# Optimization experiments

Hardware: AMD Instinct MI355X
Metric: run time of the kernel (lower is better)

Reference implementation:

```python
import jax, jax.numpy as jnp
import numpy as np

GRID_BOUND = 0.5
GRID_SIZE = 64


def _reflect(points, p):
    # points: [B, N, 3], p: [B, 4] plane (a, b, c, d) -> reflect about ax+by+cz+d=0
    n = p[:, :3]                                   # [B, 3]
    d = p[:, 3]                                    # [B]
    denom = jnp.sum(n * n, axis=-1) + 1e-12        # [B]
    t = (jnp.einsum('bnc,bc->bn', points, n) + d[:, None]) / denom[:, None]  # [B, N]
    return points - 2.0 * t[..., None] * n[:, None, :]


def _rotate(points, q):
    # points: [B, N, 3], q: [B, 4] quaternion (w, x, y, z), normalized here
    q = q / (jnp.linalg.norm(q, axis=-1, keepdims=True) + 1e-12)
    w = q[:, 0][:, None, None]                     # [B, 1, 1]
    v = q[:, 1:][:, None, :]                       # [B, 1, 3]
    uv = jnp.cross(v, points)                      # [B, N, 3]
    return points + 2.0 * jnp.cross(v, uv + w * points)


def _cal_distance(pts, cp):
    # pts: [B, N, 3]; cp: [B, G^3, 3] nearest-surface-point per voxel cell
    gs = GRID_SIZE
    # map [-gridBound, gridBound] -> voxel index in [0, gs-1]
    idx = jnp.clip(jnp.floor((pts / (2.0 * GRID_BOUND) + 0.5) * gs), 0, gs - 1).astype(jnp.int32)
    flat = (idx[..., 0] * gs + idx[..., 1]) * gs + idx[..., 2]   # [B, N]
    nearest = jnp.take_along_axis(cp, flat[..., None], axis=1)   # [B, N, 3] irregular gather
    return jnp.mean(jnp.sum((pts - nearest) ** 2, axis=-1))


def setup_inputs() -> dict:
    key = jax.random.key(0)
    k1, k2, k3, k4, k5 = jax.random.split(key, 5)
    B, N, K, gs = 128, 8192, 3, GRID_SIZE
    points = jax.random.uniform(k1, (B, N, 3), jnp.float32) - 0.5   # in [-0.5, 0.5]
    cp = jax.random.uniform(k2, (B, gs ** 3, 3), jnp.float32) - 0.5
    voxel = jax.random.uniform(k3, (B, gs, gs, gs), jnp.float32)
    plane = jax.random.normal(k4, (K, B, 4), jnp.float32)
    quat = jax.random.normal(k5, (K, B, 4), jnp.float32)
    return {"points": points, "cp": cp, "voxel": voxel, "plane": plane, "quat": quat}


def reference(points, cp, voxel, plane, quat):
    # voxel is carried for API fidelity (used only by the custom backward in the
    # original CUDA op); forward math depends on points/cp/plane/quat.
    del voxel
    # vectorize across all K symmetries instead of the original Python loop
    ref_pts = jax.vmap(_reflect, in_axes=(None, 0))(points, plane)  # [K, B, N, 3]
    rot_pts = jax.vmap(_rotate, in_axes=(None, 0))(points, quat)    # [K, B, N, 3]
    ref_loss = jnp.sum(jax.vmap(_cal_distance, in_axes=(0, None))(ref_pts, cp))
    rot_loss = jnp.sum(jax.vmap(_cal_distance, in_axes=(0, None))(rot_pts, cp))
    return ref_loss, rot_loss
```

## Files before the change

kernel.cpp:

```cpp
#include <hip/hip_runtime.h>

#define GS 64
#define BB 128
#define NN 8192
#define KK 3
#define SLICE_FLOATS (GS * GS * GS * 3)
#define B_PER_XCD 16
#define BLOCKS_PER_B 32
#define GRID (BB * BLOCKS_PER_B)

__global__ __launch_bounds__(256) void symloss_main(
    const float* __restrict__ points, const float* __restrict__ cp,
    const float* __restrict__ plane, const float* __restrict__ quat,
    float2* __restrict__ partials) {
    int raw = blockIdx.x;
    int xcd = raw & 7;
    int s   = raw >> 3;
    int b   = xcd * B_PER_XCD + s / BLOCKS_PER_B;
    int chunk = s % BLOCKS_PER_B;
    int n = chunk * 256 + threadIdx.x;

    const float* p = points + ((size_t)b * NN + n) * 3;
    float px = p[0], py = p[1], pz = p[2];
    const float* cpb = cp + (size_t)b * SLICE_FLOATS;

    float tx[2 * KK], ty[2 * KK], tz[2 * KK];

#pragma unroll
    for (int k = 0; k < KK; ++k) {
        const float* plk = plane + ((size_t)k * BB + b) * 4;
        float nx = plk[0], ny = plk[1], nz = plk[2], d = plk[3];
        float denom = nx * nx + ny * ny + nz * nz + 1e-12f;
        float tt = (px * nx + py * ny + pz * nz + d) / denom;
        tx[k] = px - 2.0f * tt * nx;
        ty[k] = py - 2.0f * tt * ny;
        tz[k] = pz - 2.0f * tt * nz;

        const float* q = quat + ((size_t)k * BB + b) * 4;
        float qw = q[0], qx = q[1], qy = q[2], qz = q[3];
        float qn = sqrtf(qw * qw + qx * qx + qy * qy + qz * qz) + 1e-12f;
        qw /= qn; qx /= qn; qy /= qn; qz /= qn;
        float ux = qy * pz - qz * py;
        float uy = qz * px - qx * pz;
        float uz = qx * py - qy * px;
        float sx = ux + qw * px;
        float sy = uy + qw * py;
        float sz = uz + qw * pz;
        tx[KK + k] = px + 2.0f * (qy * sz - qz * sy);
        ty[KK + k] = py + 2.0f * (qz * sx - qx * sz);
        tz[KK + k] = pz + 2.0f * (qx * sy - qy * sx);
    }

    const float* cptr[2 * KK];
#pragma unroll
    for (int i = 0; i < 2 * KK; ++i) {
        float fx = fminf(fmaxf(floorf((tx[i] + 0.5f) * 64.0f), 0.0f), 63.0f);
        float fy = fminf(fmaxf(floorf((ty[i] + 0.5f) * 64.0f), 0.0f), 63.0f);
        float fz = fminf(fmaxf(floorf((tz[i] + 0.5f) * 64.0f), 0.0f), 63.0f);
        int flat = (((int)fx * GS) + (int)fy) * GS + (int)fz;
        cptr[i] = cpb + (size_t)flat * 3;
    }
    float cx[2 * KK], cy[2 * KK], cz[2 * KK];
#pragma unroll
    for (int i = 0; i < 2 * KK; ++i) {
        cx[i] = cptr[i][0];
        cy[i] = cptr[i][1];
        cz[i] = cptr[i][2];
    }

    float ref_acc = 0.0f, rot_acc = 0.0f;
#pragma unroll
    for (int i = 0; i < KK; ++i) {
        float dx = tx[i] - cx[i], dy = ty[i] - cy[i], dz = tz[i] - cz[i];
        ref_acc += dx * dx + dy * dy + dz * dz;
    }
#pragma unroll
    for (int i = KK; i < 2 * KK; ++i) {
        float dx = tx[i] - cx[i], dy = ty[i] - cy[i], dz = tz[i] - cz[i];
        rot_acc += dx * dx + dy * dy + dz * dz;
    }

    for (int off = 32; off > 0; off >>= 1) {
        ref_acc += __shfl_down(ref_acc, off, 64);
        rot_acc += __shfl_down(rot_acc, off, 64);
    }
    __shared__ float s_ref[4], s_rot[4];
    int wave = threadIdx.x >> 6;
    int lane = threadIdx.x & 63;
    if (lane == 0) {
        s_ref[wave] = ref_acc;
        s_rot[wave] = rot_acc;
    }
    __syncthreads();
    if (threadIdx.x == 0) {
        float2 v;
        v.x = s_ref[0] + s_ref[1] + s_ref[2] + s_ref[3];
        v.y = s_rot[0] + s_rot[1] + s_rot[2] + s_rot[3];
        partials[blockIdx.x] = v;
    }
}

__global__ __launch_bounds__(1024) void finalize_kernel(
    const float2* __restrict__ partials, float* __restrict__ out) {
    double r = 0.0, o = 0.0;
    for (int i = threadIdx.x; i < GRID; i += 1024) {
        float2 v = partials[i];
        r += (double)v.x;
        o += (double)v.y;
    }
    __shared__ double s_r[1024], s_o[1024];
    s_r[threadIdx.x] = r;
    s_o[threadIdx.x] = o;
    __syncthreads();
    for (int off = 512; off > 0; off >>= 1) {
        if (threadIdx.x < off) {
            s_r[threadIdx.x] += s_r[threadIdx.x + off];
            s_o[threadIdx.x] += s_o[threadIdx.x + off];
        }
        __syncthreads();
    }
    if (threadIdx.x == 0) {
        const double inv = 1.0 / ((double)BB * (double)NN);
        out[0] = (float)(s_r[0] * inv);
        out[1] = (float)(s_o[0] * inv);
    }
}

extern "C" void kernel_launch(void* const* d_in, const int* in_sizes, int n_in,
                              void* d_out, int out_size, void* d_ws, size_t ws_size,
                              hipStream_t stream) {
    const float* points = (const float*)d_in[0];
    const float* cp     = (const float*)d_in[1];
    const float* plane  = (const float*)d_in[3];
    const float* quat   = (const float*)d_in[4];
    float* out = (float*)d_out;
    float2* partials = (float2*)d_ws;

    symloss_main<<<GRID, 256, 0, stream>>>(points, cp, plane, quat, partials);
    finalize_kernel<<<1, 1024, 0, stream>>>(partials, out);
}
```

Baseline: 62.30 us.

## Process two points per thread and fuse final reduction via last-block atomic

Each thread now handles two points, giving twelve independent gathers in flight per thread while halving the grid. The separate finalize kernel is removed; the last block to finish, detected with an atomic counter, reduces the partials. This removes a kernel launch and raises per-thread memory-level parallelism, at the cost of a memset launch, more registers and fewer blocks.

```diff
diff --git a/kernel.cpp b/kernel.cpp
--- a/kernel.cpp
+++ b/kernel.cpp
@@ -6,63 +6,76 @@
 #define KK 3
 #define SLICE_FLOATS (GS * GS * GS * 3)
 #define B_PER_XCD 16
-#define BLOCKS_PER_B 32
+#define BLOCKS_PER_B 16
 #define GRID (BB * BLOCKS_PER_B)
+#define NSTREAM 12
 
 __global__ __launch_bounds__(256) void symloss_main(
     const float* __restrict__ points, const float* __restrict__ cp,
     const float* __restrict__ plane, const float* __restrict__ quat,
-    float2* __restrict__ partials) {
+    float2* __restrict__ partials, unsigned* __restrict__ ctr,
+    float* __restrict__ out) {
     int raw = blockIdx.x;
     int xcd = raw & 7;
     int s   = raw >> 3;
     int b   = xcd * B_PER_XCD + s / BLOCKS_PER_B;
     int chunk = s % BLOCKS_PER_B;
-    int n = chunk * 256 + threadIdx.x;
+    int n0 = chunk * 512 + threadIdx.x;
 
-    const float* p = points + ((size_t)b * NN + n) * 3;
-    float px = p[0], py = p[1], pz = p[2];
     const float* cpb = cp + (size_t)b * SLICE_FLOATS;
 
-    float tx[2 * KK], ty[2 * KK], tz[2 * KK];
+    float px[2], py[2], pz[2];
+#pragma unroll
+    for (int t = 0; t < 2; ++t) {
+        const float* p = points + ((size_t)b * NN + n0 + t * 256) * 3;
+        px[t] = p[0]; py[t] = p[1]; pz[t] = p[2];
+    }
+
+    float tx[NSTREAM], ty[NSTREAM], tz[NSTREAM];
 
 #pragma unroll
     for (int k = 0; k < KK; ++k) {
         const float* plk = plane + ((size_t)k * BB + b) * 4;
         float nx = plk[0], ny = plk[1], nz = plk[2], d = plk[3];
         float denom = nx * nx + ny * ny + nz * nz + 1e-12f;
-        float tt = (px * nx + py * ny + pz * nz + d) / denom;
-        tx[k] = px - 2.0f * tt * nx;
-        ty[k] = py - 2.0f * tt * ny;
-        tz[k] = pz - 2.0f * tt * nz;
 
         const float* q = quat + ((size_t)k * BB + b) * 4;
         float qw = q[0], qx = q[1], qy = q[2], qz = q[3];
         float qn = sqrtf(qw * qw + qx * qx + qy * qy + qz * qz) + 1e-12f;
         qw /= qn; qx /= qn; qy /= qn; qz /= qn;
-        float ux = qy * pz - qz * py;
-        float uy = qz * px - qx * pz;
-        float uz = qx * py - qy * px;
-        float sx = ux + qw * px;
-        float sy = uy + qw * py;
-        float sz = uz + qw * pz;
-        tx[KK + k] = px + 2.0f * (qy * sz - qz * sy);
-        ty[KK + k] = py + 2.0f * (qz * sx - qx * sz);
-        tz[KK + k] = pz + 2.0f * (qx * sy - qy * sx);
+
+#pragma unroll
+        for (int t = 0; t < 2; ++t) {
+            int i = k * 2 + t;
+            float tt = (px[t] * nx + py[t] * ny + pz[t] * nz + d) / denom;
+            tx[i] = px[t] - 2.0f * tt * nx;
+            ty[i] = py[t] - 2.0f * tt * ny;
+            tz[i] = pz[t] - 2.0f * tt * nz;
+
+            float ux = qy * pz[t] - qz * py[t];
+            float uy = qz * px[t] - qx * pz[t];
+            float uz = qx * py[t] - qy * px[t];
+            float sx = ux + qw * px[t];
+            float sy = uy + qw * py[t];
+            float sz = uz + qw * pz[t];
+            tx[6 + i] = px[t] + 2.0f * (qy * sz - qz * sy);
+            ty[6 + i] = py[t] + 2.0f * (qz * sx - qx * sz);
+            tz[6 + i] = pz[t] + 2.0f * (qx * sy - qy * sx);
+        }
     }
 
-    const float* cptr[2 * KK];
+    const float* cptr[NSTREAM];
 #pragma unroll
-    for (int i = 0; i < 2 * KK; ++i) {
+    for (int i = 0; i < NSTREAM; ++i) {
         float fx = fminf(fmaxf(floorf((tx[i] + 0.5f) * 64.0f), 0.0f), 63.0f);
         float fy = fminf(fmaxf(floorf((ty[i] + 0.5f) * 64.0f), 0.0f), 63.0f);
         float fz = fminf(fmaxf(floorf((tz[i] + 0.5f) * 64.0f), 0.0f), 63.0f);
         int flat = (((int)fx * GS) + (int)fy) * GS + (int)fz;
         cptr[i] = cpb + (size_t)flat * 3;
     }
-    float cx[2 * KK], cy[2 * KK], cz[2 * KK];
+    float cx[NSTREAM], cy[NSTREAM], cz[NSTREAM];
 #pragma unroll
-    for (int i = 0; i < 2 * KK; ++i) {
+    for (int i = 0; i < NSTREAM; ++i) {
         cx[i] = cptr[i][0];
         cy[i] = cptr[i][1];
         cz[i] = cptr[i][2];
@@ -70,12 +83,12 @@
 
     float ref_acc = 0.0f, rot_acc = 0.0f;
 #pragma unroll
-    for (int i = 0; i < KK; ++i) {
+    for (int i = 0; i < 6; ++i) {
         float dx = tx[i] - cx[i], dy = ty[i] - cy[i], dz = tz[i] - cz[i];
         ref_acc += dx * dx + dy * dy + dz * dz;
     }
 #pragma unroll
-    for (int i = KK; i < 2 * KK; ++i) {
+    for (int i = 6; i < NSTREAM; ++i) {
         float dx = tx[i] - cx[i], dy = ty[i] - cy[i], dz = tz[i] - cz[i];
         rot_acc += dx * dx + dy * dy + dz * dz;
     }
@@ -92,37 +105,43 @@
         s_rot[wave] = rot_acc;
     }
     __syncthreads();
+
+    __shared__ int is_last;
     if (threadIdx.x == 0) {
         float2 v;
         v.x = s_ref[0] + s_ref[1] + s_ref[2] + s_ref[3];
         v.y = s_rot[0] + s_rot[1] + s_rot[2] + s_rot[3];
         partials[blockIdx.x] = v;
+        __threadfence();
+        unsigned old = atomicAdd(ctr, 1u);
+        is_last = (old == (unsigned)(GRID - 1));
     }
-}
+    __syncthreads();
 
-__global__ __launch_bounds__(1024) void finalize_kernel(
-    const float2* __restrict__ partials, float* __restrict__ out) {
-    double r = 0.0, o = 0.0;
-    for (int i = threadIdx.x; i < GRID; i += 1024) {
-        float2 v = partials[i];
-        r += (double)v.x;
-        o += (double)v.y;
-    }
-    __shared__ double s_r[1024], s_o[1024];
-    s_r[threadIdx.x] = r;
-    s_o[threadIdx.x] = o;
-    __syncthreads();
-    for (int off = 512; off > 0; off >>= 1) {
-        if (threadIdx.x < off) {
-            s_r[threadIdx.x] += s_r[threadIdx.x + off];
-            s_o[threadIdx.x] += s_o[threadIdx.x + off];
+    if (is_last) {
+        __threadfence();
+        double r = 0.0, o = 0.0;
+        for (int i = threadIdx.x; i < GRID; i += 256) {
+            float2 v = partials[i];
+            r += (double)v.x;
+            o += (double)v.y;
         }
+        __shared__ double d_r[256], d_o[256];
+        d_r[threadIdx.x] = r;
+        d_o[threadIdx.x] = o;
         __syncthreads();
-    }
-    if (threadIdx.x == 0) {
-        const double inv = 1.0 / ((double)BB * (double)NN);
-        out[0] = (float)(s_r[0] * inv);
-        out[1] = (float)(s_o[0] * inv);
+        for (int off = 128; off > 0; off >>= 1) {
+            if (threadIdx.x < off) {
+                d_r[threadIdx.x] += d_r[threadIdx.x + off];
+                d_o[threadIdx.x] += d_o[threadIdx.x + off];
+            }
+            __syncthreads();
+        }
+        if (threadIdx.x == 0) {
+            const double inv = 1.0 / ((double)BB * (double)NN);
+            out[0] = (float)(d_r[0] * inv);
+            out[1] = (float)(d_o[0] * inv);
+        }
     }
 }
 
@@ -134,8 +153,11 @@
     const float* plane  = (const float*)d_in[3];
     const float* quat   = (const float*)d_in[4];
     float* out = (float*)d_out;
-    float2* partials = (float2*)d_ws;
 
-    symloss_main<<<GRID, 256, 0, stream>>>(points, cp, plane, quat, partials);
-    finalize_kernel<<<1, 1024, 0, stream>>>(partials, out);
+    float2*   partials = (float2*)d_ws;
+    unsigned* ctr      = (unsigned*)((char*)d_ws + 16384);
+
+    hipMemsetAsync(ctr, 0, 4, stream);
+    symloss_main<<<GRID, 256, 0, stream>>>(points, cp, plane, quat,
+                                           partials, ctr, out);
 }
```

Measured after the change: 166.4 us. 167% more time.
